# Kernel optimization log

Measured on AMD Instinct MI355X. Metric: run time of the kernel, lower is better.

The kernel has to match this reference:

```python
import jax, jax.numpy as jnp
import numpy as np
import math

N, T, D, H = 2, 4096, 768, 12
DH = D // H


def setup_inputs() -> dict:
    key = jax.random.key(0)
    ks = jax.random.split(key, 6)
    x = jax.random.normal(ks[0], (N, T, D), dtype=jnp.float32)
    # key-padding mask: True = masked out; mask the last quarter of positions
    mask = jnp.broadcast_to(jnp.arange(T) >= (3 * T) // 4, (N, T))
    scale = 0.02
    Wq = jax.random.normal(ks[1], (D, D), dtype=jnp.float32) * scale
    Wk = jax.random.normal(ks[2], (D, D), dtype=jnp.float32) * scale
    Wv = jax.random.normal(ks[3], (D, D), dtype=jnp.float32) * scale
    Wo = jax.random.normal(ks[4], (D, D), dtype=jnp.float32) * scale
    zb = jnp.zeros((D,), dtype=jnp.float32)
    return {"x": x, "mask": mask, "Wq": Wq, "bq": zb, "Wk": Wk, "bk": zb,
            "Wv": Wv, "bv": zb, "Wo": Wo, "bo": zb}


def reference(x, mask, Wq, bq, Wk, bk, Wv, bv, Wo, bo):
    n, t, d = x.shape
    h, dh = H, d // H
    # torch Linear: y = x @ W.T + b
    def proj(W, b):
        return (x @ W.T + b).reshape(n, t, h, dh).transpose(0, 2, 1, 3)  # [n,h,t,dh]
    q = proj(Wq, bq)
    k = proj(Wk, bk)
    v = proj(Wv, bv)
    s = jnp.einsum('nhqd,nhkd->nhqk', q, k) / math.sqrt(dh)  # [n,h,t,t]
    s = jnp.where(mask[:, None, None, :], -jnp.inf, s)
    p = jax.nn.softmax(s, axis=-1)
    # dropout prob 0.0 / eval mode -> identity
    a = jnp.einsum('nhqk,nhkd->nhqd', p, v)  # [n,h,t,dh]
    a = a.transpose(0, 2, 1, 3).reshape(n, t, d)
    return a @ Wo.T + bo
```

## Files before the change

kernel.cpp:

```cpp
#include <hip/hip_runtime.h>
#include <hip/hip_bf16.h>
#include <stdint.h>

#define T_SEQ 4096
#define DM    768
#define NHEAD 12
#define DHEAD 64
#define NBAT  2
#define LOG2E 1.4426950408889634f

typedef __bf16    bf16x8 __attribute__((ext_vector_type(8)));
typedef float     f32x4  __attribute__((ext_vector_type(4)));
typedef _Float16  f16x4  __attribute__((ext_vector_type(4)));

static __device__ __forceinline__ unsigned short f2bf(float f) {
  unsigned int u = __builtin_bit_cast(unsigned int, f);
  u += 0x7FFFu + ((u >> 16) & 1u);
  return (unsigned short)(u >> 16);
}
static __device__ __forceinline__ unsigned short f2bf_hw(float f) {
  __hip_bfloat16 h = __float2bfloat16(f);
  return __builtin_bit_cast(unsigned short, h);
}
static __device__ __forceinline__ unsigned int pk2(float lo, float hi) {
  return (unsigned int)f2bf_hw(lo) | ((unsigned int)f2bf_hw(hi) << 16);
}
static __device__ __forceinline__ unsigned int pk2h(float lo, float hi) {
  unsigned short a = __builtin_bit_cast(unsigned short, (_Float16)lo);
  unsigned short b = __builtin_bit_cast(unsigned short, (_Float16)hi);
  return (unsigned int)a | ((unsigned int)b << 16);
}
static __device__ __forceinline__ void gll16(const void* g, void* l) {
  __builtin_amdgcn_global_load_lds(
      (const __attribute__((address_space(1))) unsigned int*)g,
      (__attribute__((address_space(3))) unsigned int*)l, 16, 0, 0);
}
static __device__ __forceinline__ bf16x8 ldfrag(const unsigned short* p) {
  const unsigned short* q = (const unsigned short*)__builtin_assume_aligned(p, 16);
  bf16x8 v;
  __builtin_memcpy(&v, q, 16);
  return v;
}
static __device__ __forceinline__ f16x4 ldfrag_h4(const unsigned short* p) {
  f16x4 v;
  __builtin_memcpy(&v, __builtin_assume_aligned(p, 8), 8);
  return v;
}
static __device__ __forceinline__ void st8(unsigned short* p, uint2 v) {
  __builtin_memcpy(__builtin_assume_aligned(p, 8), &v, 8);
}
static __device__ __forceinline__ uint2 ld8(const unsigned short* p) {
  uint2 v;
  __builtin_memcpy(&v, __builtin_assume_aligned(p, 8), 8);
  return v;
}

__global__ void cvt_kernel(const float* __restrict__ s, unsigned short* __restrict__ d, int n) {
  int i = (blockIdx.x * 256 + threadIdx.x) * 4;
  if (i < n) {
    float4 v = *(const float4*)(s + i);
    ushort4 o;
    o.x = f2bf(v.x); o.y = f2bf(v.y); o.z = f2bf(v.z); o.w = f2bf(v.w);
    *(ushort4*)(d + i) = o;
  }
}
__global__ void cvt4_kernel(const float* __restrict__ s0, const float* __restrict__ s1,
                            const float* __restrict__ s2, const float* __restrict__ s3,
                            unsigned short* __restrict__ d0, unsigned short* __restrict__ d1,
                            unsigned short* __restrict__ d2, unsigned short* __restrict__ d3,
                            int n) {
  int w = blockIdx.y;
  const float* sp = (w == 0) ? s0 : (w == 1) ? s1 : (w == 2) ? s2 : s3;
  unsigned short* dp = (w == 0) ? d0 : (w == 1) ? d1 : (w == 2) ? d2 : d3;
  int i = (blockIdx.x * 256 + threadIdx.x) * 4;
  if (i < n) {
    float4 v = *(const float4*)(sp + i);
    ushort4 o;
    o.x = f2bf(v.x); o.y = f2bf(v.y); o.z = f2bf(v.z); o.w = f2bf(v.w);
    *(ushort4*)(dp + i) = o;
  }
}

__global__ void init_kernel(int* __restrict__ kmx) {
  if (threadIdx.x < NBAT) { kmx[threadIdx.x] = 0; kmx[NBAT + threadIdx.x] = T_SEQ; }
}

__global__ void build_bias_kernel(const unsigned char* __restrict__ mraw,
                                  float* __restrict__ bias,
                                  int* __restrict__ kmx) {
  int idx = blockIdx.x * 256 + threadIdx.x;
  int is_u8 = (mraw[(3 * T_SEQ) / 4] != 0);
  int masked;
  if (is_u8) masked = (mraw[idx] != 0);
  else       masked = (((const int*)mraw)[idx] != 0);
  bias[idx] = masked ? -1e9f : 0.0f;
  __shared__ int smax, smin;
  if (threadIdx.x == 0) { smax = 0; smin = T_SEQ; }
  __syncthreads();
  int pos = idx & (T_SEQ - 1);
  if (!masked) atomicMax(&smax, pos + 1);
  else         atomicMin(&smin, pos);
  __syncthreads();
  if (threadIdx.x == 0) {
    atomicMax(&kmx[idx >> 12], smax);
    atomicMin(&kmx[NBAT + (idx >> 12)], smin);
  }
}

template <int MODE>
__global__ __launch_bounds__(256, (MODE == 0) ? 3 : 2) void gemm128(
    const unsigned short* __restrict__ A,
    const unsigned short* __restrict__ W0, const unsigned short* __restrict__ W1,
    const unsigned short* __restrict__ W2,
    const float* __restrict__ Bb0, const float* __restrict__ Bb1,
    const float* __restrict__ Bb2,
    void* __restrict__ O0, void* __restrict__ O1, void* __restrict__ O2) {
  constexpr int NT = (MODE == 0) ? 6 : 3;
  constexpr int NROWS = NT * 32;
  __shared__ __align__(16) unsigned short lA[128 * 64];
  __shared__ __align__(16) unsigned short lB[NROWS * 64];
  const int t = threadIdx.x;
  const int lane = t & 63, quad = lane >> 4, l16 = lane & 15;
  const int wave = t >> 6;
  const int moff = (wave & 1) * 64, noff = (wave >> 1) * (NT * 16);
  const int m0 = blockIdx.x * 128;
  const int by = blockIdx.y;
  const unsigned short* W;
  const float* Bb;
  int o0, wsel = 0;
  if constexpr (MODE == 0) {
    wsel = by >> 2;
    o0 = (by & 3) * 192;
    W  = (wsel == 0) ? W0  : ((wsel == 1) ? W1  : W2);
    Bb = (wsel == 0) ? Bb0 : ((wsel == 1) ? Bb1 : Bb2);
  } else {
    o0 = by * 96; W = W0; Bb = Bb0;
  }
  f32x4 acc[4][NT];
#pragma unroll
  for (int i = 0; i < 4; ++i)
#pragma unroll
    for (int j = 0; j < NT; ++j) acc[i][j] = (f32x4){0.f, 0.f, 0.f, 0.f};

  for (int k0 = 0; k0 < DM; k0 += 64) {
#pragma unroll
    for (int i = 0; i < 4; ++i) {
      int c = i * 256 + t;
      int r = c >> 3;
      int qc = (c & 7) ^ (r & 7);
      gll16(A + (size_t)(m0 + r) * DM + k0 + qc * 8, &lA[(i * 256 + (t & 192)) * 8]);
    }
#pragma unroll
    for (int i = 0; i < NT; ++i) {
      int c = i * 256 + t;
      int r = c >> 3;
      int qc = (c & 7) ^ (r & 7);
      gll16(W + (size_t)(o0 + r) * DM + k0 + qc * 8, &lB[(i * 256 + (t & 192)) * 8]);
    }
    __syncthreads();
    bf16x8 af[4][2];
#pragma unroll
    for (int mt = 0; mt < 4; ++mt) {
      int r = moff + mt * 16 + l16;
#pragma unroll
      for (int s = 0; s < 2; ++s)
        af[mt][s] = ldfrag(&lA[(r * 8 + ((s * 4 + quad) ^ (r & 7))) * 8]);
    }
#pragma unroll
    for (int nt = 0; nt < NT; ++nt) {
      int r = noff + nt * 16 + l16;
      bf16x8 b0 = ldfrag(&lB[(r * 8 + ((quad) ^ (r & 7))) * 8]);
      bf16x8 b1 = ldfrag(&lB[(r * 8 + ((4 + quad) ^ (r & 7))) * 8]);
#pragma unroll
      for (int mt = 0; mt < 4; ++mt) {
        acc[mt][nt] = __builtin_amdgcn_mfma_f32_16x16x32_bf16(af[mt][0], b0, acc[mt][nt], 0, 0, 0);
        acc[mt][nt] = __builtin_amdgcn_mfma_f32_16x16x32_bf16(af[mt][1], b1, acc[mt][nt], 0, 0, 0);
      }
    }
    __syncthreads();
  }
#pragma unroll
  for (int nt = 0; nt < NT; ++nt) {
    int o = o0 + noff + nt * 16 + l16;
    float bias = Bb[o];
    if (MODE == 0 && wsel == 2) {
      int h = o >> 6, d = o & 63;
#pragma unroll
      for (int mt = 0; mt < 4; ++mt) {
        int m = m0 + moff + mt * 16 + quad * 4;
        int n = m >> 12, tb = m & (T_SEQ - 1);
        uint2 w;
        w.x = pk2h(acc[mt][nt][0] + bias, acc[mt][nt][1] + bias);
        w.y = pk2h(acc[mt][nt][2] + bias, acc[mt][nt][3] + bias);
        *(uint2*)((unsigned short*)O2 +
                  ((size_t)(n * NHEAD + h) * DHEAD + d) * T_SEQ + tb) = w;
      }
      continue;
    }
#pragma unroll
    for (int mt = 0; mt < 4; ++mt) {
#pragma unroll
      for (int r = 0; r < 4; ++r) {
        int m = m0 + moff + mt * 16 + quad * 4 + r;
        float v = acc[mt][nt][r] + bias;
        if constexpr (MODE == 0) {
          int n = m >> 12, tt = m & (T_SEQ - 1);
          int h = o >> 6, d = o & 63;
          if (wsel == 0)
            ((unsigned short*)O0)[((size_t)(n * NHEAD + h) * T_SEQ + tt) * DHEAD + d] = f2bf(v * (0.125f * LOG2E));
          else
            ((unsigned short*)O1)[((size_t)(n * NHEAD + h) * T_SEQ + tt) * DHEAD + d] = f2bf(v);
        } else {
          ((float*)O0)[(size_t)m * DM + o] = v;
        }
      }
    }
  }
}

__global__ __launch_bounds__(256, 3) void flash_kernel(
    const unsigned short* __restrict__ Q, const unsigned short* __restrict__ K,
    const unsigned short* __restrict__ VT, const float* __restrict__ bias,
    const int* __restrict__ kmx, unsigned short* __restrict__ Aout) {
  __shared__ __align__(16) unsigned short lK[128 * 64];
  __shared__ __align__(16) unsigned short lV[64 * 128];
  __shared__ __align__(16) unsigned short lO[4][32 * 68];
  const int t = threadIdx.x;
  const int lane = t & 63, quad = lane >> 4, l16 = lane & 15;
  const int wave = t >> 6;
  const int b = blockIdx.x;
  const int slot = b >> 3;
  const int nh = (b & 7) * 3 + (slot % 3);
  const int q0 = (slot / 3) * 128;
  const int n = nh / NHEAD, h = nh - n * NHEAD;
  const size_t base = (size_t)nh * T_SEQ * DHEAD;

  bf16x8 qf[2][2];
#pragma unroll
  for (int qt = 0; qt < 2; ++qt) {
    int qrow = q0 + wave * 32 + qt * 16 + l16;
    qf[qt][0] = ldfrag(Q + base + (size_t)qrow * DHEAD + quad * 8);
    qf[qt][1] = ldfrag(Q + base + (size_t)qrow * DHEAD + 32 + quad * 8);
  }

  f16x4 vone_h;
#pragma unroll
  for (int i = 0; i < 4; ++i) vone_h[i] = (_Float16)1.0f;

  f32x4 oacc[2][4], oaccl[2];
#pragma unroll
  for (int qt = 0; qt < 2; ++qt) {
#pragma unroll
    for (int dt = 0; dt < 4; ++dt) oacc[qt][dt] = (f32x4){0.f, 0.f, 0.f, 0.f};
    oaccl[qt] = (f32x4){0.f, 0.f, 0.f, 0.f};
  }

  const int km = kmx[n], fm = kmx[NBAT + n];
  int ntiles = (km + 127) >> 7;
  if (ntiles > (T_SEQ >> 7)) ntiles = T_SEQ >> 7;
  const float* brow = bias + (size_t)n * T_SEQ;

  for (int it = 0; it < ntiles; ++it) {
    const int j0 = it << 7;
#pragma unroll
    for (int i = 0; i < 4; ++i) {
      int c = i * 256 + t;
      int r = c >> 3;
      int qc = (c & 7) ^ (r & 7);
      gll16(K + base + (size_t)(j0 + r) * DHEAD + qc * 8, &lK[(i * 256 + (t & 192)) * 8]);
    }
#pragma unroll
    for (int i = 0; i < 4; ++i) {
      int c = i * 256 + t;
      int r = c >> 4;
      int qc = (c & 15) ^ (r & 15);
      gll16(VT + base + (size_t)r * T_SEQ + j0 + qc * 8, &lV[(i * 256 + (t & 192)) * 8]);
    }
    __syncthreads();

    f32x4 sacc[2][8];
#pragma unroll
    for (int qt = 0; qt < 2; ++qt)
#pragma unroll
      for (int nt = 0; nt < 8; ++nt) sacc[qt][nt] = (f32x4){0.f, 0.f, 0.f, 0.f};
#pragma unroll
    for (int nt = 0; nt < 8; ++nt) {
      int r = nt * 16 + l16;
      bf16x8 k0f = ldfrag(&lK[(r * 8 + (quad ^ (r & 7))) * 8]);
      bf16x8 k1f = ldfrag(&lK[(r * 8 + ((4 + quad) ^ (r & 7))) * 8]);
#pragma unroll
      for (int qt = 0; qt < 2; ++qt) {
        sacc[qt][nt] = __builtin_amdgcn_mfma_f32_16x16x32_bf16(k0f, qf[qt][0], sacc[qt][nt], 0, 0, 0);
        sacc[qt][nt] = __builtin_amdgcn_mfma_f32_16x16x32_bf16(k1f, qf[qt][1], sacc[qt][nt], 0, 0, 0);
      }
    }
    if (j0 + 128 > fm) {
#pragma unroll
      for (int nt = 0; nt < 8; ++nt) {
        float4 bv = *(const float4*)&brow[j0 + nt * 16 + quad * 4];
#pragma unroll
        for (int qt = 0; qt < 2; ++qt) {
          sacc[qt][nt][0] += bv.x; sacc[qt][nt][1] += bv.y;
          sacc[qt][nt][2] += bv.z; sacc[qt][nt][3] += bv.w;
        }
      }
    }
    unsigned int pdh[2][8][2];
#pragma unroll
    for (int qt = 0; qt < 2; ++qt)
#pragma unroll
      for (int nt = 0; nt < 8; ++nt) {
        pdh[qt][nt][0] = pk2h(__builtin_exp2f(sacc[qt][nt][0]), __builtin_exp2f(sacc[qt][nt][1]));
        pdh[qt][nt][1] = pk2h(__builtin_exp2f(sacc[qt][nt][2]), __builtin_exp2f(sacc[qt][nt][3]));
      }
#pragma unroll
    for (int nt = 0; nt < 8; ++nt) {
      f16x4 pb[2];
#pragma unroll
      for (int qt = 0; qt < 2; ++qt) {
        uint2 u = {pdh[qt][nt][0], pdh[qt][nt][1]};
        pb[qt] = __builtin_bit_cast(f16x4, u);
      }
#pragma unroll
      for (int dt = 0; dt < 4; ++dt) {
        int rv = dt * 16 + l16;
        int swz = (nt * 2 + (quad >> 1)) ^ l16;
        f16x4 vf = ldfrag_h4(&lV[(rv * 16 + swz) * 8 + (quad & 1) * 4]);
#pragma unroll
        for (int qt = 0; qt < 2; ++qt)
          oacc[qt][dt] = __builtin_amdgcn_mfma_f32_16x16x16f16(vf, pb[qt], oacc[qt][dt], 0, 0, 0);
      }
#pragma unroll
      for (int qt = 0; qt < 2; ++qt)
        oaccl[qt] = __builtin_amdgcn_mfma_f32_16x16x16f16(vone_h, pb[qt], oaccl[qt], 0, 0, 0);
    }
    __syncthreads();
  }
  unsigned short* lOw = lO[wave];
#pragma unroll
  for (int qt = 0; qt < 2; ++qt) {
    float l = oaccl[qt][0];
    float rl = (l > 0.f) ? 1.0f / l : 0.f;
#pragma unroll
    for (int dt = 0; dt < 4; ++dt) {
      uint2 w;
      w.x = pk2(oacc[qt][dt][0] * rl, oacc[qt][dt][1] * rl);
      w.y = pk2(oacc[qt][dt][2] * rl, oacc[qt][dt][3] * rl);
      st8(lOw + (qt * 16 + l16) * 68 + dt * 16 + quad * 4, w);
    }
  }
#pragma unroll
  for (int it2 = 0; it2 < 8; ++it2) {
    int rowq = it2 * 4 + quad;
    uint2 w = ld8(lOw + rowq * 68 + l16 * 4);
    int tt = q0 + wave * 32 + rowq;
    *(uint2*)(Aout + (size_t)(n * T_SEQ + tt) * DM + h * DHEAD + l16 * 4) = w;
  }
}

extern "C" void kernel_launch(void* const* d_in, const int* in_sizes, int n_in,
                              void* d_out, int out_size, void* d_ws, size_t ws_size,
                              hipStream_t stream) {
  const float*         x  = (const float*)d_in[0];
  const unsigned char* mk = (const unsigned char*)d_in[1];
  const float* Wq = (const float*)d_in[2];
  const float* bq = (const float*)d_in[3];
  const float* Wk = (const float*)d_in[4];
  const float* bk = (const float*)d_in[5];
  const float* Wv = (const float*)d_in[6];
  const float* bv = (const float*)d_in[7];
  const float* Wo = (const float*)d_in[8];
  const float* bo = (const float*)d_in[9];

  const int xe = NBAT * T_SEQ * DM;
  const int we = DM * DM;
  const size_t xb_bytes = (size_t)xe * 2;
  const size_t wb_bytes = (size_t)we * 2;
  const size_t kv_bytes = (size_t)NBAT * NHEAD * T_SEQ * DHEAD * 2;

  auto rnd = [](size_t b) { return (b + 255) & ~(size_t)255; };
  size_t need = rnd(xb_bytes) + 4 * rnd(wb_bytes) + 2 * rnd(kv_bytes) +
                rnd((size_t)NBAT * T_SEQ * 4) + 256;
  if (ws_size < need) return;

  char* ws = (char*)d_ws;
  size_t off = 0;
  auto alloc = [&](size_t b) { char* p = ws + off; off += rnd(b); return p; };
  unsigned short* x_b  = (unsigned short*)alloc(xb_bytes);
  unsigned short* wq_b = (unsigned short*)alloc(wb_bytes);
  unsigned short* wk_b = (unsigned short*)alloc(wb_bytes);
  unsigned short* wv_b = (unsigned short*)alloc(wb_bytes);
  unsigned short* wo_b = (unsigned short*)alloc(wb_bytes);
  unsigned short* k_ws  = (unsigned short*)alloc(kv_bytes);
  unsigned short* vt_ws = (unsigned short*)alloc(kv_bytes);
  float* bias = (float*)alloc((size_t)NBAT * T_SEQ * 4);
  int* kmx    = (int*)alloc(256);
  unsigned short* q_ws = (unsigned short*)d_out;
  unsigned short* a_ws = x_b;

  init_kernel<<<1, 64, 0, stream>>>(kmx);
  cvt_kernel<<<xe / 1024, 256, 0, stream>>>(x, x_b, xe);
  cvt4_kernel<<<dim3(we / 1024, 4), 256, 0, stream>>>(
      Wq, Wk, Wv, Wo, wq_b, wk_b, wv_b, wo_b, we);
  build_bias_kernel<<<(NBAT * T_SEQ) / 256, 256, 0, stream>>>(mk, bias, kmx);
  gemm128<0><<<dim3((NBAT * T_SEQ) / 128, 12), 256, 0, stream>>>(
      x_b, wq_b, wk_b, wv_b, bq, bk, bv, q_ws, k_ws, vt_ws);
  flash_kernel<<<NBAT * NHEAD * (T_SEQ / 128), 256, 0, stream>>>(
      q_ws, k_ws, vt_ws, bias, kmx, a_ws);
  gemm128<1><<<dim3((NBAT * T_SEQ) / 128, 8), 256, 0, stream>>>(
      a_ws, wo_b, wo_b, wo_b, bo, bo, bo, d_out, d_out, d_out);
  (void)in_sizes; (void)n_in; (void)out_size;
}
```

Before: 290.4 us.

## Double-buffer 64-key K/V tiles in LDS and stream the softmax per subtile

Shrinks the flash-attention key tile from 128 to 64 and double-buffers K and V^T in a single shared array, so the async global-to-LDS load of the next tile overlaps compute on the current one, with one barrier per iteration instead of two. The inner loop is restructured to compute scores, exponentiate and accumulate P·V per 16-key subtile rather than materialising the whole score block, which lowers register pressure. The output staging buffer is aliased onto the same LDS. The trade-off is twice as many loop iterations and barriers, a new swizzle for the narrower V tile, and the risk that the in-flight prefetch is not fully waited on before the barrier.

```diff
diff --git a/kernel.cpp b/kernel.cpp
--- a/kernel.cpp
+++ b/kernel.cpp
@@ -222,9 +222,7 @@
     const unsigned short* __restrict__ Q, const unsigned short* __restrict__ K,
     const unsigned short* __restrict__ VT, const float* __restrict__ bias,
     const int* __restrict__ kmx, unsigned short* __restrict__ Aout) {
-  __shared__ __align__(16) unsigned short lK[128 * 64];
-  __shared__ __align__(16) unsigned short lV[64 * 128];
-  __shared__ __align__(16) unsigned short lO[4][32 * 68];
+  __shared__ __align__(16) unsigned short smem[16384];
   const int t = threadIdx.x;
   const int lane = t & 63, quad = lane >> 4, l16 = lane & 15;
   const int wave = t >> 6;
@@ -256,87 +254,77 @@
   }
 
   const int km = kmx[n], fm = kmx[NBAT + n];
-  int ntiles = (km + 127) >> 7;
-  if (ntiles > (T_SEQ >> 7)) ntiles = T_SEQ >> 7;
+  int ntiles = (km + 63) >> 6;
+  if (ntiles > (T_SEQ >> 6)) ntiles = T_SEQ >> 6;
   const float* brow = bias + (size_t)n * T_SEQ;
 
-  for (int it = 0; it < ntiles; ++it) {
-    const int j0 = it << 7;
-#pragma unroll
-    for (int i = 0; i < 4; ++i) {
+  auto stage = [&](int j0, int buf) {
+#pragma unroll
+    for (int i = 0; i < 2; ++i) {
       int c = i * 256 + t;
       int r = c >> 3;
       int qc = (c & 7) ^ (r & 7);
-      gll16(K + base + (size_t)(j0 + r) * DHEAD + qc * 8, &lK[(i * 256 + (t & 192)) * 8]);
-    }
-#pragma unroll
-    for (int i = 0; i < 4; ++i) {
+      gll16(K + base + (size_t)(j0 + r) * DHEAD + qc * 8,
+            &smem[buf * 4096 + (i * 256 + (t & 192)) * 8]);
+    }
+#pragma unroll
+    for (int i = 0; i < 2; ++i) {
       int c = i * 256 + t;
-      int r = c >> 4;
-      int qc = (c & 15) ^ (r & 15);
-      gll16(VT + base + (size_t)r * T_SEQ + j0 + qc * 8, &lV[(i * 256 + (t & 192)) * 8]);
-    }
+      int r = c >> 3;
+      int qc = (c & 7) ^ (r & 7);
+      gll16(VT + base + (size_t)r * T_SEQ + j0 + qc * 8,
+            &smem[8192 + buf * 4096 + (i * 256 + (t & 192)) * 8]);
+    }
+  };
+
+  stage(0, 0);
+
+  for (int it = 0; it < ntiles; ++it) {
+    const int j0 = it << 6;
+    const int buf = it & 1;
     __syncthreads();
-
-    f32x4 sacc[2][8];
-#pragma unroll
-    for (int qt = 0; qt < 2; ++qt)
-#pragma unroll
-      for (int nt = 0; nt < 8; ++nt) sacc[qt][nt] = (f32x4){0.f, 0.f, 0.f, 0.f};
-#pragma unroll
-    for (int nt = 0; nt < 8; ++nt) {
+    if (it + 1 < ntiles) stage((it + 1) << 6, buf ^ 1);
+    const unsigned short* lKb = &smem[buf * 4096];
+    const unsigned short* lVb = &smem[8192 + buf * 4096];
+    const bool touch = (j0 + 64 > fm);
+
+#pragma unroll
+    for (int nt = 0; nt < 4; ++nt) {
       int r = nt * 16 + l16;
-      bf16x8 k0f = ldfrag(&lK[(r * 8 + (quad ^ (r & 7))) * 8]);
-      bf16x8 k1f = ldfrag(&lK[(r * 8 + ((4 + quad) ^ (r & 7))) * 8]);
-#pragma unroll
-      for (int qt = 0; qt < 2; ++qt) {
-        sacc[qt][nt] = __builtin_amdgcn_mfma_f32_16x16x32_bf16(k0f, qf[qt][0], sacc[qt][nt], 0, 0, 0);
-        sacc[qt][nt] = __builtin_amdgcn_mfma_f32_16x16x32_bf16(k1f, qf[qt][1], sacc[qt][nt], 0, 0, 0);
+      bf16x8 k0f = ldfrag(&lKb[(r * 8 + (quad ^ (r & 7))) * 8]);
+      bf16x8 k1f = ldfrag(&lKb[(r * 8 + ((4 + quad) ^ (r & 7))) * 8]);
+      f32x4 s0 = (f32x4){0.f, 0.f, 0.f, 0.f};
+      f32x4 s1 = (f32x4){0.f, 0.f, 0.f, 0.f};
+      s0 = __builtin_amdgcn_mfma_f32_16x16x32_bf16(k0f, qf[0][0], s0, 0, 0, 0);
+      s0 = __builtin_amdgcn_mfma_f32_16x16x32_bf16(k1f, qf[0][1], s0, 0, 0, 0);
+      s1 = __builtin_amdgcn_mfma_f32_16x16x32_bf16(k0f, qf[1][0], s1, 0, 0, 0);
+      s1 = __builtin_amdgcn_mfma_f32_16x16x32_bf16(k1f, qf[1][1], s1, 0, 0, 0);
+      if (touch) {
+        float4 bv = *(const float4*)&brow[j0 + nt * 16 + quad * 4];
+        s0[0] += bv.x; s0[1] += bv.y; s0[2] += bv.z; s0[3] += bv.w;
+        s1[0] += bv.x; s1[1] += bv.y; s1[2] += bv.z; s1[3] += bv.w;
       }
-    }
-    if (j0 + 128 > fm) {
-#pragma unroll
-      for (int nt = 0; nt < 8; ++nt) {
-        float4 bv = *(const float4*)&brow[j0 + nt * 16 + quad * 4];
-#pragma unroll
-        for (int qt = 0; qt < 2; ++qt) {
-          sacc[qt][nt][0] += bv.x; sacc[qt][nt][1] += bv.y;
-          sacc[qt][nt][2] += bv.z; sacc[qt][nt][3] += bv.w;
-        }
-      }
-    }
-    unsigned int pdh[2][8][2];
-#pragma unroll
-    for (int qt = 0; qt < 2; ++qt)
-#pragma unroll
-      for (int nt = 0; nt < 8; ++nt) {
-        pdh[qt][nt][0] = pk2h(__builtin_exp2f(sacc[qt][nt][0]), __builtin_exp2f(sacc[qt][nt][1]));
-        pdh[qt][nt][1] = pk2h(__builtin_exp2f(sacc[qt][nt][2]), __builtin_exp2f(sacc[qt][nt][3]));
-      }
-#pragma unroll
-    for (int nt = 0; nt < 8; ++nt) {
-      f16x4 pb[2];
-#pragma unroll
-      for (int qt = 0; qt < 2; ++qt) {
-        uint2 u = {pdh[qt][nt][0], pdh[qt][nt][1]};
-        pb[qt] = __builtin_bit_cast(f16x4, u);
-      }
+      uint2 u0, u1;
+      u0.x = pk2h(__builtin_exp2f(s0[0]), __builtin_exp2f(s0[1]));
+      u0.y = pk2h(__builtin_exp2f(s0[2]), __builtin_exp2f(s0[3]));
+      u1.x = pk2h(__builtin_exp2f(s1[0]), __builtin_exp2f(s1[1]));
+      u1.y = pk2h(__builtin_exp2f(s1[2]), __builtin_exp2f(s1[3]));
+      f16x4 pb0 = __builtin_bit_cast(f16x4, u0);
+      f16x4 pb1 = __builtin_bit_cast(f16x4, u1);
 #pragma unroll
       for (int dt = 0; dt < 4; ++dt) {
         int rv = dt * 16 + l16;
-        int swz = (nt * 2 + (quad >> 1)) ^ l16;
-        f16x4 vf = ldfrag_h4(&lV[(rv * 16 + swz) * 8 + (quad & 1) * 4]);
-#pragma unroll
-        for (int qt = 0; qt < 2; ++qt)
-          oacc[qt][dt] = __builtin_amdgcn_mfma_f32_16x16x16f16(vf, pb[qt], oacc[qt][dt], 0, 0, 0);
+        int swz = (nt * 2 + (quad >> 1)) ^ (rv & 7);
+        f16x4 vf = ldfrag_h4(&lVb[(rv * 8 + swz) * 8 + (quad & 1) * 4]);
+        oacc[0][dt] = __builtin_amdgcn_mfma_f32_16x16x16f16(vf, pb0, oacc[0][dt], 0, 0, 0);
+        oacc[1][dt] = __builtin_amdgcn_mfma_f32_16x16x16f16(vf, pb1, oacc[1][dt], 0, 0, 0);
       }
-#pragma unroll
-      for (int qt = 0; qt < 2; ++qt)
-        oaccl[qt] = __builtin_amdgcn_mfma_f32_16x16x16f16(vone_h, pb[qt], oaccl[qt], 0, 0, 0);
-    }
-    __syncthreads();
-  }
-  unsigned short* lOw = lO[wave];
+      oaccl[0] = __builtin_amdgcn_mfma_f32_16x16x16f16(vone_h, pb0, oaccl[0], 0, 0, 0);
+      oaccl[1] = __builtin_amdgcn_mfma_f32_16x16x16f16(vone_h, pb1, oaccl[1], 0, 0, 0);
+    }
+  }
+  __syncthreads();
+  unsigned short* lOw = &smem[wave * 2176];
 #pragma unroll
   for (int qt = 0; qt < 2; ++qt) {
     float l = oaccl[qt][0];
```

Measured after the change: 276.6 us. 4.7% less time.
